# Kernel optimization log

Measured on AMD Instinct MI355X. Metric: run time of the kernel, lower is better.

Reference implementation:

```python
import jax, jax.numpy as jnp
import numpy as np

N_NODES = 100000
D_FEAT = 64
HIDDEN = 64
N_CLASSES = 16
N_EDGES = 1600000


def setup_inputs() -> dict:
    key = jax.random.key(0)
    ks = jax.random.split(key, 8)
    x = jax.random.normal(ks[0], (N_NODES, D_FEAT), dtype=jnp.float32)
    edge_index = jax.random.randint(ks[1], (2, N_EDGES), 0, N_NODES, dtype=jnp.int64)
    s1 = 1.0 / np.sqrt(D_FEAT)
    s2 = 1.0 / np.sqrt(HIDDEN)
    W1 = jax.random.uniform(ks[2], (D_FEAT, HIDDEN), jnp.float32, -s1, s1)
    b1 = jnp.zeros((HIDDEN,), jnp.float32)
    W2 = jax.random.uniform(ks[3], (HIDDEN, HIDDEN), jnp.float32, -s2, s2)
    b2 = jnp.zeros((HIDDEN,), jnp.float32)
    Wfc = jax.random.uniform(ks[4], (HIDDEN, N_CLASSES), jnp.float32, -s2, s2)
    bfc = jax.random.uniform(ks[5], (N_CLASSES,), jnp.float32, -s2, s2)
    return {"x": x, "edge_index": edge_index, "W1": W1, "b1": b1,
            "W2": W2, "b2": b2, "Wfc": Wfc, "bfc": bfc}


def reference(x, edge_index, W1, b1, W2, b2, Wfc, bfc):
    N = x.shape[0]
    loops = jnp.arange(N, dtype=edge_index.dtype)
    # GCNConv adds self-loops by default
    src = jnp.concatenate([edge_index[0], loops])  # message source j
    dst = jnp.concatenate([edge_index[1], loops])  # aggregation target i
    # symmetric normalization: D^{-1/2} (A + I) D^{-1/2}, degree counted on targets
    deg = jax.ops.segment_sum(jnp.ones_like(dst, dtype=x.dtype), dst, num_segments=N)
    dinv = jnp.where(deg > 0, jax.lax.rsqrt(deg), 0.0)
    norm = dinv[src] * dinv[dst]  # [E+N]

    def gcn_conv(h, W, b):
        h = h @ W                              # [N, out] dense transform first (PyG order)
        msg = h[src] * norm[:, None]            # gather + edge scaling, [E+N, out]
        return jax.ops.segment_sum(msg, dst, num_segments=N) + b

    h = jax.nn.relu(gcn_conv(x, W1, b1))
    # dropout is identity in eval mode
    h = jax.nn.relu(gcn_conv(h, W2, b2))
    return jax.nn.softmax(h @ Wfc + bfc, axis=1)
```

## Files before the change

kernel.cpp:

```cpp
#include <hip/hip_runtime.h>
#include <hip/hip_fp16.h>
#include <math.h>

#define NNODES 100000
#define BSHIFT 7
#define BSIZE 128
#define NBUCK ((NNODES + BSIZE - 1) >> BSHIFT)
#define SCAT_BLOCKS 512
#define CHUNKCAP 3328
#define CAPSHIFT 12
#define BCAP (1 << CAPSHIFT)

__global__ __launch_bounds__(1024) void k_init(int* __restrict__ bcur) {
    int k = blockIdx.x * 1024 + threadIdx.x;
    if (k < NBUCK) bcur[k] = k << CAPSHIFT;
}

__global__ __launch_bounds__(256) void k_scatter_fused(const int* __restrict__ src, const int* __restrict__ dst,
                                                       int* __restrict__ bcur, int* __restrict__ staging,
                                                       int E, int chunk) {
    __shared__ int epack[CHUNKCAP];
    __shared__ unsigned short ebuck[CHUNKCAP];
    __shared__ int hist[NBUCK];
    __shared__ int lcur[NBUCK];
    int t = threadIdx.x;
    for (int k = t; k < NBUCK; k += 256) hist[k] = 0;
    __syncthreads();
    int c0 = blockIdx.x * chunk;
    int c1 = min(E, c0 + chunk);
    int n = c1 - c0;
    for (int j = t; j < n; j += 256) {
        int d = dst[c0 + j];
        int s = src[c0 + j];
        int b = d >> BSHIFT;
        epack[j] = (s << BSHIFT) | (d & (BSIZE - 1));
        ebuck[j] = (unsigned short)b;
        atomicAdd(&hist[b], 1);
    }
    __syncthreads();
    for (int k = t; k < NBUCK; k += 256) {
        int c = hist[k];
        lcur[k] = c ? atomicAdd(&bcur[k], c) : 0;
    }
    __syncthreads();
    for (int j = t; j < n; j += 256) {
        int pos = atomicAdd(&lcur[ebuck[j]], 1);
        staging[pos] = epack[j];
    }
}

__global__ __launch_bounds__(256) void k_bucket_csr(const int* __restrict__ staging, const int* __restrict__ bcur,
                                                    int* __restrict__ rowptr, int* __restrict__ rowend,
                                                    int* __restrict__ ssoff, float* __restrict__ dinv, int N) {
    __shared__ int lcnt[BSIZE], lpre[BSIZE];
    int b = blockIdx.x, t = threadIdx.x;
    int node0 = b << BSHIFT;
    int bbase = b << CAPSHIFT;
    int bend = bcur[b];
    if (t < BSIZE) lcnt[t] = 0;
    __syncthreads();
    for (int e = bbase + t; e < bend; e += 256)
        atomicAdd(&lcnt[staging[e] & (BSIZE - 1)], 1);
    __syncthreads();
    if (t < BSIZE) lpre[t] = lcnt[t];
    __syncthreads();
    #pragma unroll
    for (int off = 1; off < BSIZE; off <<= 1) {
        int u = 0;
        if (t < BSIZE && t >= off) u = lpre[t - off];
        __syncthreads();
        if (t < BSIZE) lpre[t] += u;
        __syncthreads();
    }
    if (t < BSIZE) {
        int node = node0 + t;
        if (node < N) {
            int beg = bbase + lpre[t] - lcnt[t];
            rowptr[node] = beg;
            rowend[node] = beg + lcnt[t];
            dinv[node] = rsqrtf((float)(lcnt[t] + 1));
        }
        lpre[t] -= lcnt[t];
    }
    __syncthreads();
    for (int e = bbase + t; e < bend; e += 256) {
        int p = staging[e];
        int pos = atomicAdd(&lpre[p & (BSIZE - 1)], 1);
        ssoff[bbase + pos] = (p >> BSHIFT) << 7;
    }
}

__global__ __launch_bounds__(256) void k_transform3(const float* __restrict__ X, const float* __restrict__ W,
                                                    const float* __restrict__ dinv, __half* __restrict__ Gh, int N) {
    __shared__ float4 Xs[2048];
    __shared__ float dinvs[128];
    int t = threadIdx.x;
    int lane = t & 63;
    int node0 = blockIdx.x << 7;
    {
        const float4* X4 = (const float4*)X;
        int lim4 = N << 4;
        int gbase = node0 << 4;
        #pragma unroll
        for (int j = 0; j < 8; j++) {
            int f = j * 256 + t;
            int gi = gbase + f;
            Xs[f] = (gi < lim4) ? X4[gi] : make_float4(0.f, 0.f, 0.f, 0.f);
        }
    }
    if (t < 128) {
        int nd = node0 + t;
        dinvs[t] = (nd < N) ? dinv[nd] : 0.f;
    }
    float w[64];
    #pragma unroll
    for (int k = 0; k < 64; k++) w[k] = W[k * 64 + lane];
    __syncthreads();
    int woff = (t >> 6) * 32;
    for (int nn = 0; nn < 32; nn += 4) {
        const float4* r0 = &Xs[(woff + nn + 0) * 16];
        const float4* r1 = &Xs[(woff + nn + 1) * 16];
        const float4* r2 = &Xs[(woff + nn + 2) * 16];
        const float4* r3 = &Xs[(woff + nn + 3) * 16];
        float a0 = 0.f, a1 = 0.f, a2 = 0.f, a3 = 0.f;
        #pragma unroll
        for (int kq = 0; kq < 16; kq++) {
            float4 xa = r0[kq];
            float4 xb = r1[kq];
            float4 xc = r2[kq];
            float4 xd = r3[kq];
            a0 = fmaf(xa.x, w[4*kq+0], a0); a0 = fmaf(xa.y, w[4*kq+1], a0);
            a0 = fmaf(xa.z, w[4*kq+2], a0); a0 = fmaf(xa.w, w[4*kq+3], a0);
            a1 = fmaf(xb.x, w[4*kq+0], a1); a1 = fmaf(xb.y, w[4*kq+1], a1);
            a1 = fmaf(xb.z, w[4*kq+2], a1); a1 = fmaf(xb.w, w[4*kq+3], a1);
            a2 = fmaf(xc.x, w[4*kq+0], a2); a2 = fmaf(xc.y, w[4*kq+1], a2);
            a2 = fmaf(xc.z, w[4*kq+2], a2); a2 = fmaf(xc.w, w[4*kq+3], a2);
            a3 = fmaf(xd.x, w[4*kq+0], a3); a3 = fmaf(xd.y, w[4*kq+1], a3);
            a3 = fmaf(xd.z, w[4*kq+2], a3); a3 = fmaf(xd.w, w[4*kq+3], a3);
        }
        int nb = node0 + woff + nn;
        float d0 = dinvs[woff+nn+0], d1 = dinvs[woff+nn+1];
        float d2 = dinvs[woff+nn+2], d3 = dinvs[woff+nn+3];
        if (nb + 3 < N) {
            Gh[(size_t)(nb+0)*64 + lane] = __float2half(a0 * d0);
            Gh[(size_t)(nb+1)*64 + lane] = __float2half(a1 * d1);
            Gh[(size_t)(nb+2)*64 + lane] = __float2half(a2 * d2);
            Gh[(size_t)(nb+3)*64 + lane] = __float2half(a3 * d3);
        } else {
            if (nb+0 < N) Gh[(size_t)(nb+0)*64 + lane] = __float2half(a0 * d0);
            if (nb+1 < N) Gh[(size_t)(nb+1)*64 + lane] = __float2half(a1 * d1);
            if (nb+2 < N) Gh[(size_t)(nb+2)*64 + lane] = __float2half(a2 * d2);
            if (nb+3 < N) Gh[(size_t)(nb+3)*64 + lane] = __float2half(a3 * d3);
        }
    }
}

__global__ __launch_bounds__(256) void k_agg(const __half* __restrict__ G, const int* __restrict__ rowptr,
                                             const int* __restrict__ rowend, const int* __restrict__ ssoff,
                                             const float* __restrict__ dinv, const float* __restrict__ bias,
                                             float* __restrict__ O, int N) {
    int lane = threadIdx.x & 63;
    int wid = threadIdx.x >> 6;
    int sub = lane >> 3;
    int l = lane & 7;
    int i = blockIdx.x * 4 + wid;
    if (i >= N) return;
    const char* Gb = (const char*)G;
    int loff = l << 4;
    int beg = rowptr[i], end = rowend[i];
    float a[8] = {0.f, 0.f, 0.f, 0.f, 0.f, 0.f, 0.f, 0.f};
    int e = beg + sub;
    for (; e + 8 < end; e += 16) {
        int o0 = ssoff[e];
        int o1 = ssoff[e + 8];
        float4 g0 = *(const float4*)(Gb + o0 + loff);
        float4 g1 = *(const float4*)(Gb + o1 + loff);
        const __half2* h0 = (const __half2*)&g0;
        const __half2* h1 = (const __half2*)&g1;
        #pragma unroll
        for (int q = 0; q < 4; q++) {
            __half2 s = __hadd2(h0[q], h1[q]);
            float2 f = __half22float2(s);
            a[2 * q]     += f.x;
            a[2 * q + 1] += f.y;
        }
    }
    if (e < end) {
        int o0 = ssoff[e];
        float4 g0 = *(const float4*)(Gb + o0 + loff);
        const __half2* h0 = (const __half2*)&g0;
        #pragma unroll
        for (int q = 0; q < 4; q++) {
            float2 f0 = __half22float2(h0[q]);
            a[2 * q]     += f0.x;
            a[2 * q + 1] += f0.y;
        }
    }
    #pragma unroll
    for (int mask = 8; mask <= 32; mask <<= 1) {
        #pragma unroll
        for (int q = 0; q < 8; q++) a[q] += __shfl_xor(a[q], mask);
    }
    if (sub == 0) {
        float4 gs = *(const float4*)(Gb + (i << 7) + loff);
        const __half2* hs = (const __half2*)&gs;
        #pragma unroll
        for (int q = 0; q < 4; q++) {
            float2 fs = __half22float2(hs[q]);
            a[2 * q]     += fs.x;
            a[2 * q + 1] += fs.y;
        }
        float di = dinv[i];
        float4 b0 = *(const float4*)(bias + 8 * l);
        float4 b1 = *(const float4*)(bias + 8 * l + 4);
        float4 o0v, o1v;
        o0v.x = fmaxf(fmaf(di, a[0], b0.x), 0.f);
        o0v.y = fmaxf(fmaf(di, a[1], b0.y), 0.f);
        o0v.z = fmaxf(fmaf(di, a[2], b0.z), 0.f);
        o0v.w = fmaxf(fmaf(di, a[3], b0.w), 0.f);
        o1v.x = fmaxf(fmaf(di, a[4], b1.x), 0.f);
        o1v.y = fmaxf(fmaf(di, a[5], b1.y), 0.f);
        o1v.z = fmaxf(fmaf(di, a[6], b1.z), 0.f);
        o1v.w = fmaxf(fmaf(di, a[7], b1.w), 0.f);
        *(float4*)(O + (size_t)i * 64 + 8 * l) = o0v;
        *(float4*)(O + (size_t)i * 64 + 8 * l + 4) = o1v;
    }
}

__global__ __launch_bounds__(256) void k_fc_softmax(const float* __restrict__ H, const float* __restrict__ Wfc,
                                                    const float* __restrict__ bfc, float* __restrict__ O, int N) {
    __shared__ float wf[64 * 16];
    __shared__ float bf[16];
    int t = threadIdx.x;
    for (int k = t; k < 1024; k += 256) wf[k] = Wfc[k];
    if (t < 16) bf[t] = bfc[t];
    __syncthreads();
    int gid = blockIdx.x * 256 + t;
    int node = gid >> 4;
    int c = gid & 15;
    if (node >= N) return;
    const float4* hv = (const float4*)(H + (size_t)node * 64);
    float acc = bf[c];
    #pragma unroll
    for (int kk = 0; kk < 16; kk++) {
        float4 h4 = hv[kk];
        acc = fmaf(h4.x, wf[(4 * kk + 0) * 16 + c], acc);
        acc = fmaf(h4.y, wf[(4 * kk + 1) * 16 + c], acc);
        acc = fmaf(h4.z, wf[(4 * kk + 2) * 16 + c], acc);
        acc = fmaf(h4.w, wf[(4 * kk + 3) * 16 + c], acc);
    }
    float m = acc;
    #pragma unroll
    for (int mask = 1; mask < 16; mask <<= 1) m = fmaxf(m, __shfl_xor(m, mask));
    float ex = expf(acc - m);
    float s = ex;
    #pragma unroll
    for (int mask = 1; mask < 16; mask <<= 1) s += __shfl_xor(s, mask);
    O[(size_t)node * 16 + c] = ex / s;
}

extern "C" void kernel_launch(void* const* d_in, const int* in_sizes, int n_in,
                              void* d_out, int out_size, void* d_ws, size_t ws_size,
                              hipStream_t stream) {
    const float* x   = (const float*)d_in[0];
    const int*   ei  = (const int*)d_in[1];
    const float* W1  = (const float*)d_in[2];
    const float* b1  = (const float*)d_in[3];
    const float* W2  = (const float*)d_in[4];
    const float* b2  = (const float*)d_in[5];
    const float* Wfc = (const float*)d_in[6];
    const float* bfc = (const float*)d_in[7];
    float* out = (float*)d_out;
    const int N = NNODES;
    const int E = in_sizes[1] / 2;

    char* ws = (char*)d_ws;
    size_t off = 0;
    auto take = [&](size_t bytes) {
        char* p = ws + off;
        off = (off + bytes + 255) & ~(size_t)255;
        return p;
    };
    int*    staging = (int*)take((size_t)NBUCK * BCAP * 4);
    int*    ssoff   = (int*)take((size_t)NBUCK * BCAP * 4);
    float*  bufB    = (float*)take((size_t)N * 64 * 4);
    __half* Gh      = (__half*)take((size_t)N * 64 * 2);
    int*    rowptr  = (int*)take((size_t)N * 4);
    int*    rowend  = (int*)take((size_t)N * 4);
    float*  dinv    = (float*)take((size_t)N * 4);
    int*    bcur    = (int*)take((size_t)NBUCK * 4);

    const int* e_src = ei;
    const int* e_dst = ei + E;

    int chunk = (E + SCAT_BLOCKS - 1) / SCAT_BLOCKS;
    k_init<<<1, 1024, 0, stream>>>(bcur);
    k_scatter_fused<<<SCAT_BLOCKS, 256, 0, stream>>>(e_src, e_dst, bcur, staging, E, chunk);
    k_bucket_csr<<<NBUCK, 256, 0, stream>>>(staging, bcur, rowptr, rowend, ssoff, dinv, N);

    int tb = (N + 127) / 128;
    k_transform3<<<tb, 256, 0, stream>>>(x, W1, dinv, Gh, N);
    k_agg<<<(N + 3) / 4, 256, 0, stream>>>(Gh, rowptr, rowend, ssoff, dinv, b1, bufB, N);
    k_transform3<<<tb, 256, 0, stream>>>(bufB, W2, dinv, Gh, N);
    k_agg<<<(N + 3) / 4, 256, 0, stream>>>(Gh, rowptr, rowend, ssoff, dinv, b2, bufB, N);
    k_fc_softmax<<<(N * 16 + 255) / 256, 256, 0, stream>>>(bufB, Wfc, bfc, out, N);
}
```

Baseline: 210.4 us.

## Fuse CSR build with first transform and FC-softmax into second aggregation

Replaces the bucket-cursor init kernel with a memset and makes cursors relative offsets. Merges the bucket CSR build with the first-layer dense transform, since both use 128-node blocks, so dinv comes straight from shared memory. Folds the final FC plus softmax into the second aggregation kernel, which removes a separate kernel and the 25.6 MB write and re-read of hidden activations. Reworks the aggregation loop so each 8-lane group gathers 4 contiguous edges per iteration, trading more registers for memory-level parallelism.

```diff
diff --git a/kernel.cpp b/kernel.cpp
--- a/kernel.cpp
+++ b/kernel.cpp
@@ -10,11 +10,6 @@
 #define CHUNKCAP 3328
 #define CAPSHIFT 12
 #define BCAP (1 << CAPSHIFT)
-
-__global__ __launch_bounds__(1024) void k_init(int* __restrict__ bcur) {
-    int k = blockIdx.x * 1024 + threadIdx.x;
-    if (k < NBUCK) bcur[k] = k << CAPSHIFT;
-}
 
 __global__ __launch_bounds__(256) void k_scatter_fused(const int* __restrict__ src, const int* __restrict__ dst,
                                                        int* __restrict__ bcur, int* __restrict__ staging,
@@ -40,7 +35,8 @@
     __syncthreads();
     for (int k = t; k < NBUCK; k += 256) {
         int c = hist[k];
-        lcur[k] = c ? atomicAdd(&bcur[k], c) : 0;
+        int ofs = c ? atomicAdd(&bcur[k], c) : 0;
+        lcur[k] = (k << CAPSHIFT) + ofs;
     }
     __syncthreads();
     for (int j = t; j < n; j += 256) {
@@ -49,14 +45,19 @@
     }
 }
 
-__global__ __launch_bounds__(256) void k_bucket_csr(const int* __restrict__ staging, const int* __restrict__ bcur,
-                                                    int* __restrict__ rowptr, int* __restrict__ rowend,
-                                                    int* __restrict__ ssoff, float* __restrict__ dinv, int N) {
+__global__ __launch_bounds__(256) void k_csr_transform(const int* __restrict__ staging, const int* __restrict__ bcur,
+                                                       int* __restrict__ rowptr, int* __restrict__ rowend,
+                                                       int* __restrict__ ssoff, float* __restrict__ dinv,
+                                                       const float* __restrict__ X, const float* __restrict__ W,
+                                                       __half* __restrict__ Gh, int N) {
+    __shared__ float4 Xs[2048];
+    __shared__ float dinvs[128];
     __shared__ int lcnt[BSIZE], lpre[BSIZE];
     int b = blockIdx.x, t = threadIdx.x;
+    int lane = t & 63;
     int node0 = b << BSHIFT;
     int bbase = b << CAPSHIFT;
-    int bend = bcur[b];
+    int bend = bbase + bcur[b];
     if (t < BSIZE) lcnt[t] = 0;
     __syncthreads();
     for (int e = bbase + t; e < bend; e += 256)
@@ -74,11 +75,13 @@
     }
     if (t < BSIZE) {
         int node = node0 + t;
+        float dv = rsqrtf((float)(lcnt[t] + 1));
+        dinvs[t] = dv;
         if (node < N) {
             int beg = bbase + lpre[t] - lcnt[t];
             rowptr[node] = beg;
             rowend[node] = beg + lcnt[t];
-            dinv[node] = rsqrtf((float)(lcnt[t] + 1));
+            dinv[node] = dv;
         }
         lpre[t] -= lcnt[t];
     }
@@ -88,15 +91,6 @@
         int pos = atomicAdd(&lpre[p & (BSIZE - 1)], 1);
         ssoff[bbase + pos] = (p >> BSHIFT) << 7;
     }
-}
-
-__global__ __launch_bounds__(256) void k_transform3(const float* __restrict__ X, const float* __restrict__ W,
-                                                    const float* __restrict__ dinv, __half* __restrict__ Gh, int N) {
-    __shared__ float4 Xs[2048];
-    __shared__ float dinvs[128];
-    int t = threadIdx.x;
-    int lane = t & 63;
-    int node0 = blockIdx.x << 7;
     {
         const float4* X4 = (const float4*)X;
         int lim4 = N << 4;
@@ -107,10 +101,6 @@
             int gi = gbase + f;
             Xs[f] = (gi < lim4) ? X4[gi] : make_float4(0.f, 0.f, 0.f, 0.f);
         }
-    }
-    if (t < 128) {
-        int nd = node0 + t;
-        dinvs[t] = (nd < N) ? dinv[nd] : 0.f;
     }
     float w[64];
     #pragma unroll
@@ -155,12 +145,88 @@
     }
 }
 
-__global__ __launch_bounds__(256) void k_agg(const __half* __restrict__ G, const int* __restrict__ rowptr,
-                                             const int* __restrict__ rowend, const int* __restrict__ ssoff,
-                                             const float* __restrict__ dinv, const float* __restrict__ bias,
-                                             float* __restrict__ O, int N) {
-    int lane = threadIdx.x & 63;
-    int wid = threadIdx.x >> 6;
+__global__ __launch_bounds__(256) void k_transform3(const float* __restrict__ X, const float* __restrict__ W,
+                                                    const float* __restrict__ dinv, __half* __restrict__ Gh, int N) {
+    __shared__ float4 Xs[2048];
+    __shared__ float dinvs[128];
+    int t = threadIdx.x;
+    int lane = t & 63;
+    int node0 = blockIdx.x << 7;
+    {
+        const float4* X4 = (const float4*)X;
+        int lim4 = N << 4;
+        int gbase = node0 << 4;
+        #pragma unroll
+        for (int j = 0; j < 8; j++) {
+            int f = j * 256 + t;
+            int gi = gbase + f;
+            Xs[f] = (gi < lim4) ? X4[gi] : make_float4(0.f, 0.f, 0.f, 0.f);
+        }
+    }
+    if (t < 128) {
+        int nd = node0 + t;
+        dinvs[t] = (nd < N) ? dinv[nd] : 0.f;
+    }
+    float w[64];
+    #pragma unroll
+    for (int k = 0; k < 64; k++) w[k] = W[k * 64 + lane];
+    __syncthreads();
+    int woff = (t >> 6) * 32;
+    for (int nn = 0; nn < 32; nn += 4) {
+        const float4* r0 = &Xs[(woff + nn + 0) * 16];
+        const float4* r1 = &Xs[(woff + nn + 1) * 16];
+        const float4* r2 = &Xs[(woff + nn + 2) * 16];
+        const float4* r3 = &Xs[(woff + nn + 3) * 16];
+        float a0 = 0.f, a1 = 0.f, a2 = 0.f, a3 = 0.f;
+        #pragma unroll
+        for (int kq = 0; kq < 16; kq++) {
+            float4 xa = r0[kq];
+            float4 xb = r1[kq];
+            float4 xc = r2[kq];
+            float4 xd = r3[kq];
+            a0 = fmaf(xa.x, w[4*kq+0], a0); a0 = fmaf(xa.y, w[4*kq+1], a0);
+            a0 = fmaf(xa.z, w[4*kq+2], a0); a0 = fmaf(xa.w, w[4*kq+3], a0);
+            a1 = fmaf(xb.x, w[4*kq+0], a1); a1 = fmaf(xb.y, w[4*kq+1], a1);
+            a1 = fmaf(xb.z, w[4*kq+2], a1); a1 = fmaf(xb.w, w[4*kq+3], a1);
+            a2 = fmaf(xc.x, w[4*kq+0], a2); a2 = fmaf(xc.y, w[4*kq+1], a2);
+            a2 = fmaf(xc.z, w[4*kq+2], a2); a2 = fmaf(xc.w, w[4*kq+3], a2);
+            a3 = fmaf(xd.x, w[4*kq+0], a3); a3 = fmaf(xd.y, w[4*kq+1], a3);
+            a3 = fmaf(xd.z, w[4*kq+2], a3); a3 = fmaf(xd.w, w[4*kq+3], a3);
+        }
+        int nb = node0 + woff + nn;
+        float d0 = dinvs[woff+nn+0], d1 = dinvs[woff+nn+1];
+        float d2 = dinvs[woff+nn+2], d3 = dinvs[woff+nn+3];
+        if (nb + 3 < N) {
+            Gh[(size_t)(nb+0)*64 + lane] = __float2half(a0 * d0);
+            Gh[(size_t)(nb+1)*64 + lane] = __float2half(a1 * d1);
+            Gh[(size_t)(nb+2)*64 + lane] = __float2half(a2 * d2);
+            Gh[(size_t)(nb+3)*64 + lane] = __float2half(a3 * d3);
+        } else {
+            if (nb+0 < N) Gh[(size_t)(nb+0)*64 + lane] = __float2half(a0 * d0);
+            if (nb+1 < N) Gh[(size_t)(nb+1)*64 + lane] = __float2half(a1 * d1);
+            if (nb+2 < N) Gh[(size_t)(nb+2)*64 + lane] = __float2half(a2 * d2);
+            if (nb+3 < N) Gh[(size_t)(nb+3)*64 + lane] = __float2half(a3 * d3);
+        }
+    }
+}
+
+template<bool FC>
+__global__ __launch_bounds__(256) void k_agg_t(const __half* __restrict__ G, const int* __restrict__ rowptr,
+                                               const int* __restrict__ rowend, const int* __restrict__ ssoff,
+                                               const float* __restrict__ dinv, const float* __restrict__ bias,
+                                               const float* __restrict__ Wfc, const float* __restrict__ bfc,
+                                               float* __restrict__ O, int N) {
+    __shared__ float wf[1024];
+    __shared__ float wfb[16];
+    int t = threadIdx.x;
+    if (FC) {
+        #pragma unroll
+        for (int k = 0; k < 4; k++) wf[k * 256 + t] = Wfc[k * 256 + t];
+        if (t < 16) wfb[t] = bfc[t];
+        __syncthreads();
+    }
+    int lane = t & 63;
+    int wid = t >> 6;
     int sub = lane >> 3;
     int l = lane & 7;
     int i = blockIdx.x * 4 + wid;
@@ -169,31 +235,62 @@
     int loff = l << 4;
     int beg = rowptr[i], end = rowend[i];
     float a[8] = {0.f, 0.f, 0.f, 0.f, 0.f, 0.f, 0.f, 0.f};
-    int e = beg + sub;
-    for (; e + 8 < end; e += 16) {
-        int o0 = ssoff[e];
-        int o1 = ssoff[e + 8];
+    int e = beg;
+    for (; e + 32 <= end; e += 32) {
+        int b0 = e + 4 * sub;
+        int o0 = ssoff[b0], o1 = ssoff[b0 + 1], o2 = ssoff[b0 + 2], o3 = ssoff[b0 + 3];
+        float4 g0 = *(const float4*)(Gb + o0 + loff);
+        float4 g1 = *(const float4*)(Gb + o1 + loff);
+        float4 g2 = *(const float4*)(Gb + o2 + loff);
+        float4 g3 = *(const float4*)(Gb + o3 + loff);
+        const __half2* h0 = (const __half2*)&g0;
+        const __half2* h1 = (const __half2*)&g1;
+        const __half2* h2 = (const __half2*)&g2;
+        const __half2* h3 = (const __half2*)&g3;
+        #pragma unroll
+        for (int q = 0; q < 4; q++) {
+            float2 fA = __half22float2(__hadd2(h0[q], h1[q]));
+            float2 fB = __half22float2(__hadd2(h2[q], h3[q]));
+            a[2 * q]     += fA.x + fB.x;
+            a[2 * q + 1] += fA.y + fB.y;
+        }
+    }
+    if (e + 16 <= end) {
+        int b0 = e + 2 * sub;
+        int o0 = ssoff[b0], o1 = ssoff[b0 + 1];
         float4 g0 = *(const float4*)(Gb + o0 + loff);
         float4 g1 = *(const float4*)(Gb + o1 + loff);
         const __half2* h0 = (const __half2*)&g0;
         const __half2* h1 = (const __half2*)&g1;
         #pragma unroll
         for (int q = 0; q < 4; q++) {
-            __half2 s = __hadd2(h0[q], h1[q]);
-            float2 f = __half22float2(s);
+            float2 f = __half22float2(__hadd2(h0[q], h1[q]));
             a[2 * q]     += f.x;
             a[2 * q + 1] += f.y;
         }
-    }
-    if (e < end) {
-        int o0 = ssoff[e];
+        e += 16;
+    }
+    if (e + 8 <= end) {
+        int o0 = ssoff[e + sub];
         float4 g0 = *(const float4*)(Gb + o0 + loff);
         const __half2* h0 = (const __half2*)&g0;
         #pragma unroll
         for (int q = 0; q < 4; q++) {
-            float2 f0 = __half22float2(h0[q]);
-            a[2 * q]     += f0.x;
-            a[2 * q + 1] += f0.y;
+            float2 f = __half22float2(h0[q]);
+            a[2 * q]     += f.x;
+            a[2 * q + 1] += f.y;
+        }
+        e += 8;
+    }
+    if (e + sub < end) {
+        int o0 = ssoff[e + sub];
+        float4 g0 = *(const float4*)(Gb + o0 + loff);
+        const __half2* h0 = (const __half2*)&g0;
+        #pragma unroll
+        for (int q = 0; q < 4; q++) {
+            float2 f = __half22float2(h0[q]);
+            a[2 * q]     += f.x;
+            a[2 * q + 1] += f.y;
         }
     }
     #pragma unroll
@@ -201,62 +298,52 @@
         #pragma unroll
         for (int q = 0; q < 8; q++) a[q] += __shfl_xor(a[q], mask);
     }
-    if (sub == 0) {
-        float4 gs = *(const float4*)(Gb + (i << 7) + loff);
-        const __half2* hs = (const __half2*)&gs;
-        #pragma unroll
-        for (int q = 0; q < 4; q++) {
-            float2 fs = __half22float2(hs[q]);
-            a[2 * q]     += fs.x;
-            a[2 * q + 1] += fs.y;
-        }
-        float di = dinv[i];
-        float4 b0 = *(const float4*)(bias + 8 * l);
-        float4 b1 = *(const float4*)(bias + 8 * l + 4);
-        float4 o0v, o1v;
-        o0v.x = fmaxf(fmaf(di, a[0], b0.x), 0.f);
-        o0v.y = fmaxf(fmaf(di, a[1], b0.y), 0.f);
-        o0v.z = fmaxf(fmaf(di, a[2], b0.z), 0.f);
-        o0v.w = fmaxf(fmaf(di, a[3], b0.w), 0.f);
-        o1v.x = fmaxf(fmaf(di, a[4], b1.x), 0.f);
-        o1v.y = fmaxf(fmaf(di, a[5], b1.y), 0.f);
-        o1v.z = fmaxf(fmaf(di, a[6], b1.z), 0.f);
-        o1v.w = fmaxf(fmaf(di, a[7], b1.w), 0.f);
-        *(float4*)(O + (size_t)i * 64 + 8 * l) = o0v;
-        *(float4*)(O + (size_t)i * 64 + 8 * l + 4) = o1v;
-    }
-}
-
-__global__ __launch_bounds__(256) void k_fc_softmax(const float* __restrict__ H, const float* __restrict__ Wfc,
-                                                    const float* __restrict__ bfc, float* __restrict__ O, int N) {
-    __shared__ float wf[64 * 16];
-    __shared__ float bf[16];
-    int t = threadIdx.x;
-    for (int k = t; k < 1024; k += 256) wf[k] = Wfc[k];
-    if (t < 16) bf[t] = bfc[t];
-    __syncthreads();
-    int gid = blockIdx.x * 256 + t;
-    int node = gid >> 4;
-    int c = gid & 15;
-    if (node >= N) return;
-    const float4* hv = (const float4*)(H + (size_t)node * 64);
-    float acc = bf[c];
-    #pragma unroll
-    for (int kk = 0; kk < 16; kk++) {
-        float4 h4 = hv[kk];
-        acc = fmaf(h4.x, wf[(4 * kk + 0) * 16 + c], acc);
-        acc = fmaf(h4.y, wf[(4 * kk + 1) * 16 + c], acc);
-        acc = fmaf(h4.z, wf[(4 * kk + 2) * 16 + c], acc);
-        acc = fmaf(h4.w, wf[(4 * kk + 3) * 16 + c], acc);
-    }
-    float m = acc;
-    #pragma unroll
-    for (int mask = 1; mask < 16; mask <<= 1) m = fmaxf(m, __shfl_xor(m, mask));
-    float ex = expf(acc - m);
-    float s = ex;
-    #pragma unroll
-    for (int mask = 1; mask < 16; mask <<= 1) s += __shfl_xor(s, mask);
-    O[(size_t)node * 16 + c] = ex / s;
+    float4 gs = *(const float4*)(Gb + (i << 7) + loff);
+    const __half2* hs = (const __half2*)&gs;
+    float di = dinv[i];
+    float4 b0v = *(const float4*)(bias + 8 * l);
+    float4 b1v = *(const float4*)(bias + 8 * l + 4);
+    float bb[8] = {b0v.x, b0v.y, b0v.z, b0v.w, b1v.x, b1v.y, b1v.z, b1v.w};
+    float r[8];
+    #pragma unroll
+    for (int q = 0; q < 4; q++) {
+        float2 fs = __half22float2(hs[q]);
+        r[2 * q]     = fmaxf(fmaf(di, a[2 * q] + fs.x, bb[2 * q]), 0.f);
+        r[2 * q + 1] = fmaxf(fmaf(di, a[2 * q + 1] + fs.y, bb[2 * q + 1]), 0.f);
+    }
+    if (!FC) {
+        if (sub == 0) {
+            *(float4*)(O + (size_t)i * 64 + 8 * l)     = make_float4(r[0], r[1], r[2], r[3]);
+            *(float4*)(O + (size_t)i * 64 + 8 * l + 4) = make_float4(r[4], r[5], r[6], r[7]);
+        }
+    } else {
+        int c0 = 2 * sub;
+        float p0 = 0.f, p1 = 0.f;
+        #pragma unroll
+        for (int q = 0; q < 8; q++) {
+            int f = 8 * l + q;
+            p0 = fmaf(r[q], wf[f * 16 + c0], p0);
+            p1 = fmaf(r[q], wf[f * 16 + c0 + 1], p1);
+        }
+        #pragma unroll
+        for (int mask = 1; mask <= 4; mask <<= 1) {
+            p0 += __shfl_xor(p0, mask);
+            p1 += __shfl_xor(p1, mask);
+        }
+        p0 += wfb[c0];
+        p1 += wfb[c0 + 1];
+        float mx = fmaxf(p0, p1);
+        #pragma unroll
+        for (int mask = 8; mask <= 32; mask <<= 1) mx = fmaxf(mx, __shfl_xor(mx, mask));
+        float e0 = expf(p0 - mx), e1 = expf(p1 - mx);
+        float ssum = e0 + e1;
+        #pragma unroll
+        for (int mask = 8; mask <= 32; mask <<= 1) ssum += __shfl_xor(ssum, mask);
+        if (l == 0) {
+            float inv = 1.0f / ssum;
+            *(float2*)(O + (size_t)i * 16 + c0) = make_float2(e0 * inv, e1 * inv);
+        }
+    }
 }
 
 extern "C" void kernel_launch(void* const* d_in, const int* in_sizes, int n_in,
@@ -294,14 +381,12 @@
     const int* e_dst = ei + E;
 
     int chunk = (E + SCAT_BLOCKS - 1) / SCAT_BLOCKS;
-    k_init<<<1, 1024, 0, stream>>>(bcur);
+    hipMemsetAsync(bcur, 0, (size_t)NBUCK * 4, stream);
     k_scatter_fused<<<SCAT_BLOCKS, 256, 0, stream>>>(e_src, e_dst, bcur, staging, E, chunk);
-    k_bucket_csr<<<NBUCK, 256, 0, stream>>>(staging, bcur, rowptr, rowend, ssoff, dinv, N);
-
-    int tb = (N + 127) / 128;
-    k_transform3<<<tb, 256, 0, stream>>>(x, W1, dinv, Gh, N);
-    k_agg<<<(N + 3) / 4, 256, 0, stream>>>(Gh, rowptr, rowend, ssoff, dinv, b1, bufB, N);
-    k_transform3<<<tb, 256, 0, stream>>>(bufB, W2, dinv, Gh, N);
-    k_agg<<<(N + 3) / 4, 256, 0, stream>>>(Gh, rowptr, rowend, ssoff, dinv, b2, bufB, N);
-    k_fc_softmax<<<(N * 16 + 255) / 256, 256, 0, stream>>>(bufB, Wfc, bfc, out, N);
-}
+    k_csr_transform<<<NBUCK, 256, 0, stream>>>(staging, bcur, rowptr, rowend, ssoff, dinv, x, W1, Gh, N);
+    k_agg_t<false><<<(N + 3) / 4, 256, 0, stream>>>(Gh, rowptr, rowend, ssoff, dinv, b1,
+                                                    nullptr, nullptr, bufB, N);
+    k_transform3<<<(N + 127) / 128, 256, 0, stream>>>(bufB, W2, dinv, Gh, N);
+    k_agg_t<true><<<(N + 3) / 4, 256, 0, stream>>>(Gh, rowptr, rowend, ssoff, dinv, b2,
+                                                   Wfc, bfc, out, N);
+}
```

Measured after the change: 244.1 us. 16.0% more time.
